# Performance work log

Measured on AMD Instinct MI355X. Metric: run time of the kernel, lower is better.

Reference implementation:

```python
import jax, jax.numpy as jnp
import numpy as np
import math

B, T, C, N = 2, 2048, 1024, 16  # batch, seq, h_dim, n_heads
D = C // N                      # head dim = 64


def setup_inputs() -> dict:
    key = jax.random.key(0)
    ks = jax.random.split(key, 9)
    s = 1.0 / math.sqrt(C)
    x = jax.random.normal(ks[0], (B, T, C), dtype=jnp.float32)
    Wq = jax.random.normal(ks[1], (C, C), dtype=jnp.float32) * s
    Wk = jax.random.normal(ks[2], (C, C), dtype=jnp.float32) * s
    Wv = jax.random.normal(ks[3], (C, C), dtype=jnp.float32) * s
    Wp = jax.random.normal(ks[4], (C, C), dtype=jnp.float32) * s
    bq = jax.random.normal(ks[5], (C,), dtype=jnp.float32) * 0.01
    bk = jax.random.normal(ks[6], (C,), dtype=jnp.float32) * 0.01
    bv = jax.random.normal(ks[7], (C,), dtype=jnp.float32) * 0.01
    bp = jax.random.normal(ks[8], (C,), dtype=jnp.float32) * 0.01
    mask = jnp.tril(jnp.ones((T, T), dtype=jnp.int32))[None, None]  # [1,1,T,T] causal
    return {"x": x, "Wq": Wq, "bq": bq, "Wk": Wk, "bk": bk,
            "Wv": Wv, "bv": bv, "Wp": Wp, "bp": bp, "mask": mask}


def reference(x, Wq, bq, Wk, bk, Wv, bv, Wp, bp, mask):
    b, t, c = x.shape
    n, d = N, c // N
    # projections; rearrange 'b t (n d) -> b n t d'
    q = (x @ Wq + bq).reshape(b, t, n, d).transpose(0, 2, 1, 3)
    k = (x @ Wk + bk).reshape(b, t, n, d).transpose(0, 2, 1, 3)
    v = (x @ Wv + bv).reshape(b, t, n, d).transpose(0, 2, 1, 3)
    # source: (q @ k^T).transpose(2,3) -> weights[b,n,i,j] = q_j . k_i (TRANSPOSED scores)
    weights = jnp.einsum('bntd,bnsd->bnst', q, k) / math.sqrt(d)
    weights = jnp.where(mask == 0, -jnp.inf, weights)
    attn = jax.nn.softmax(weights, axis=-1)          # softmax over query index j
    out = jnp.einsum('bnij,bnjd->bnid', attn, v)     # [b,n,t,d]
    out = out.transpose(0, 2, 1, 3).reshape(b, t, c)
    return out @ Wp + bp
```

## Files before the change

### kernel.cpp

```cpp
#include <hip/hip_runtime.h>
#include <hip/hip_bf16.h>

#define TT 2048

typedef __attribute__((ext_vector_type(8))) short bf16x8;
typedef __attribute__((ext_vector_type(4))) float f32x4;
typedef __attribute__((ext_vector_type(8))) unsigned short us8;
typedef __attribute__((ext_vector_type(4))) unsigned short us4;

typedef __attribute__((address_space(1))) void gvoid;
typedef __attribute__((address_space(3))) void svoid;

__device__ __forceinline__ void gll16(const void* g, void* l) {
    __builtin_amdgcn_global_load_lds((gvoid*)g, (svoid*)l, 16, 0, 0);
}

__device__ __forceinline__ unsigned short f2bf(float f) {
    union { float f; unsigned u; } v; v.f = f;
    unsigned r = v.u + 0x7fffu + ((v.u >> 16) & 1u);
    return (unsigned short)(r >> 16);
}
__device__ __forceinline__ float bf2f(unsigned short u) {
    union { unsigned u; float f; } v; v.u = ((unsigned)u) << 16;
    return v.f;
}

#define MFMA16(a, b, c) __builtin_amdgcn_mfma_f32_16x16x32_bf16((a), (b), (c), 0, 0, 0)

__global__ __launch_bounds__(256) void convert_x(const float* __restrict__ x,
                                                 unsigned short* __restrict__ xh,
                                                 unsigned short* __restrict__ xl) {
    const int i = blockIdx.x * 256 + threadIdx.x;
    const float4 a = ((const float4*)x)[2 * i];
    const float4 b = ((const float4*)x)[2 * i + 1];
    const float v[8] = {a.x, a.y, a.z, a.w, b.x, b.y, b.z, b.w};
    us8 H, L;
    #pragma unroll
    for (int j = 0; j < 8; ++j) {
        const unsigned short h = f2bf(v[j]);
        H[j] = h;
        L[j] = f2bf(v[j] - bf2f(h));
    }
    ((us8*)xh)[i] = H;
    ((us8*)xl)[i] = L;
}

__global__ __launch_bounds__(256) void convert_w(const float* __restrict__ W,
                                                 unsigned short* __restrict__ Wh,
                                                 unsigned short* __restrict__ Wl) {
    __shared__ float tile[32 * 33];
    const int t = threadIdx.x;
    const int k0 = blockIdx.x * 32, n0 = blockIdx.y * 32;

    const int kl_ = t >> 3, nc = (t & 7) * 4;
    const float4 v = *(const float4*)&W[(size_t)(k0 + kl_) * 1024 + n0 + nc];
    tile[(nc + 0) * 33 + kl_] = v.x;
    tile[(nc + 1) * 33 + kl_] = v.y;
    tile[(nc + 2) * 33 + kl_] = v.z;
    tile[(nc + 3) * 33 + kl_] = v.w;
    __syncthreads();
    const int nl = t >> 3, kc = (t & 7) * 4;
    us4 H, L;
    #pragma unroll
    for (int j = 0; j < 4; ++j) {
        const float f = tile[nl * 33 + kc + j];
        const unsigned short h = f2bf(f);
        H[j] = h;
        L[j] = f2bf(f - bf2f(h));
    }
    *(us4*)&Wh[(size_t)(n0 + nl) * 1024 + k0 + kc] = H;
    *(us4*)&Wl[(size_t)(n0 + nl) * 1024 + k0 + kc] = L;
}

template <int BM, int OUTMODE>
__global__ __launch_bounds__(256, 2)
void proj2(const unsigned short* __restrict__ Ah, const unsigned short* __restrict__ Al,
           const unsigned short* __restrict__ Bh, const unsigned short* __restrict__ Bl,
           const float* __restrict__ bias0, const float* __restrict__ bias1,
           unsigned short* __restrict__ Oh, unsigned short* __restrict__ Ol,
           float* __restrict__ Of) {
    constexpr int MT = BM / 32;
    constexpr int RW = BM / 2;
    constexpr int CA = BM / 64;
    __shared__ __align__(16) unsigned short sm[BM * 64 + 8192];
    unsigned short* sAh = sm;
    unsigned short* sAl = sm + BM * 32;
    unsigned short* sBh = sm + BM * 64;
    unsigned short* sBl = sm + BM * 64 + 4096;

    const int t = threadIdx.x;
    const int lane = t & 63, w = t >> 6;
    const int wr = w >> 1, wc = w & 1;
    const int l15 = lane & 15, lq = lane >> 4;

    const int nwg = gridDim.x * gridDim.y;
    const int bid = blockIdx.y * gridDim.x + blockIdx.x;
    const int swz = (bid & 7) * (nwg >> 3) + (bid >> 3);
    const int bx = swz % gridDim.x, by = swz / gridDim.x;
    const int row0 = bx * BM;
    const int col0 = by * 128;

    f32x4 acc[MT][4] = {};

    for (int k0 = 0; k0 < 1024; k0 += 32) {
        __syncthreads();
        #pragma unroll
        for (int cc = 0; cc < CA; ++cc) {
            const int c = w * CA + cc;
            const int r = c * 16 + (lane >> 2);
            const int src = (row0 + r) * 1024 + k0 + 8 * ((lane & 3) ^ ((r >> 1) & 3));
            gll16(&Ah[src], &sAh[c * 512]);
            gll16(&Al[src], &sAl[c * 512]);
        }
        #pragma unroll
        for (int cc = 0; cc < 2; ++cc) {
            const int c = w * 2 + cc;
            const int r = c * 16 + (lane >> 2);
            const int src = (col0 + r) * 1024 + k0 + 8 * ((lane & 3) ^ ((r >> 1) & 3));
            gll16(&Bh[src], &sBh[c * 512]);
            gll16(&Bl[src], &sBl[c * 512]);
        }
        __syncthreads();

        bf16x8 aH[MT], aL[MT], bH[4], bL[4];
        #pragma unroll
        for (int nt = 0; nt < 4; ++nt) {
            const int rn = 64 * wc + 16 * nt + l15;
            const int off = rn * 32 + 8 * (lq ^ ((rn >> 1) & 3));
            bH[nt] = *(const bf16x8*)&sBh[off];
            bL[nt] = *(const bf16x8*)&sBl[off];
        }
        #pragma unroll
        for (int mt = 0; mt < MT; ++mt) {
            const int rm = RW * wr + 16 * mt + l15;
            const int off = rm * 32 + 8 * (lq ^ ((rm >> 1) & 3));
            aH[mt] = *(const bf16x8*)&sAh[off];
            aL[mt] = *(const bf16x8*)&sAl[off];
        }
        #pragma unroll
        for (int mt = 0; mt < MT; ++mt)
            #pragma unroll
            for (int nt = 0; nt < 4; ++nt) {
                acc[mt][nt] = MFMA16(aH[mt], bH[nt], acc[mt][nt]);
                acc[mt][nt] = MFMA16(aH[mt], bL[nt], acc[mt][nt]);
                acc[mt][nt] = MFMA16(aL[mt], bH[nt], acc[mt][nt]);
            }
    }

    if (OUTMODE == 3) {
        __syncthreads();
        unsigned short* sv = sm;
        #pragma unroll
        for (int mt = 0; mt < MT; ++mt)
            #pragma unroll
            for (int nt = 0; nt < 4; ++nt) {
                const int cl = 64 * wc + 16 * nt + l15;
                const float bb = bias0[col0 + cl];
                #pragma unroll
                for (int r = 0; r < 4; ++r) {
                    const int tl = RW * wr + 16 * mt + 4 * lq + r;
                    sv[cl * 72 + tl] = f2bf(acc[mt][nt][r] + bb);
                }
            }
        __syncthreads();
        const int b = row0 >> 11, t0 = row0 & 2047;
        #pragma unroll
        for (int it = 0; it < 4; ++it) {
            const int cl = it * 32 + (t >> 3);
            const int ts = (t & 7) * 8;
            const us8 o8 = *(const us8*)&sv[cl * 72 + ts];
            const int c = col0 + cl;
            *(us8*)&Oh[((size_t)((b * 16 + (c >> 6)) * 64 + (c & 63))) * 2048 + t0 + ts] = o8;
        }
        return;
    }

    __syncthreads();
    float* sc = (float*)sm + w * (RW * 32);
    #pragma unroll
    for (int h = 0; h < 2; ++h) {
        #pragma unroll
        for (int mt = 0; mt < MT; ++mt)
            #pragma unroll
            for (int nt2 = 0; nt2 < 2; ++nt2) {
                const int nt = 2 * h + nt2;
                const int colg = col0 + 64 * wc + 16 * nt + l15;
                float bb;
                if (OUTMODE == 0) bb = (col0 < 1024) ? bias0[colg] : bias1[colg - 1024];
                else bb = bias0[colg];
                const int cl = 16 * nt2 + l15;
                #pragma unroll
                for (int r = 0; r < 4; ++r) {
                    const int row = 16 * mt + 4 * lq + r;
                    sc[row * 32 + 4 * ((cl >> 2) ^ (row & 7)) + (cl & 3)] = acc[mt][nt][r] + bb;
                }
            }
        asm volatile("" ::: "memory");
        #pragma unroll
        for (int it = 0; it < RW / 16; ++it) {
            const int rl = it * 16 + (lane >> 2);
            const int c8 = (lane & 3) * 8;
            const float4 f0 = *(const float4*)&sc[rl * 32 + 4 * ((c8 >> 2) ^ (rl & 7))];
            const float4 f1 = *(const float4*)&sc[rl * 32 + 4 * (((c8 >> 2) + 1) ^ (rl & 7))];
            const int gr = row0 + RW * wr + rl;
            const int gc = col0 + 64 * wc + 32 * h + c8;
            if (OUTMODE == 2) {
                *(float4*)&Of[(size_t)gr * 1024 + gc] = f0;
                *(float4*)&Of[(size_t)gr * 1024 + gc + 4] = f1;
            } else {
                const float v[8] = {f0.x, f0.y, f0.z, f0.w, f1.x, f1.y, f1.z, f1.w};
                us8 H, L;
                #pragma unroll
                for (int j = 0; j < 8; ++j) {
                    const unsigned short hh = f2bf(v[j]);
                    H[j] = hh;
                    L[j] = f2bf(v[j] - bf2f(hh));
                }
                *(us8*)&Oh[(size_t)gr * 2048 + gc] = H;
                *(us8*)&Ol[(size_t)gr * 2048 + gc] = L;
            }
        }
        asm volatile("" ::: "memory");
    }
}

__global__ __launch_bounds__(256, 2)
void attn2(const unsigned short* __restrict__ QKh, const unsigned short* __restrict__ QKl,
           const unsigned short* __restrict__ Vt,
           unsigned short* __restrict__ Oh, unsigned short* __restrict__ Ol) {
    __shared__ __align__(16) unsigned short sm[20480];
    unsigned short* sQh = sm;
    unsigned short* sQl = sm + 4096;
    unsigned short* sKh = sm + 8192;
    unsigned short* sKl = sm + 12288;
    unsigned short* sVt = sm + 16384;
    unsigned short* sP  = sm;

    const int t = threadIdx.x;
    const int lane = t & 63, w = t >> 6;
    const int l15 = lane & 15, lq = lane >> 4;
    const int bn = blockIdx.x;
    const int b = bn >> 4, n = bn & 15;
    const int qt = (gridDim.y - 1) - blockIdx.y;
    const int rowQ0 = b * TT + qt * 64;
    const int colQ = 1024 + n * 64;
    const int colK = n * 64;

    #pragma unroll
    for (int cc = 0; cc < 2; ++cc) {
        const int c = w * 2 + cc;
        const int r = 8 * c + (lane >> 3);
        const int src = (rowQ0 + r) * 2048 + colQ + 8 * ((lane & 7) ^ (r & 7));
        gll16(&QKh[src], &sQh[c * 512]);
        gll16(&QKl[src], &sQl[c * 512]);
    }
    __syncthreads();
    bf16x8 qH[2], qL[2];
    #pragma unroll
    for (int kh = 0; kh < 2; ++kh) {
        const int rq = 16 * w + l15;
        const int off = rq * 64 + 8 * ((lq + 4 * kh) ^ (rq & 7));
        qH[kh] = *(const bf16x8*)&sQh[off];
        qL[kh] = *(const bf16x8*)&sQl[off];
    }

    float m_[4], l_[4];
    f32x4 o[4] = {};
    #pragma unroll
    for (int r = 0; r < 4; ++r) { m_[r] = -1e30f; l_[r] = 0.f; }

    for (int kt = 0; kt <= qt; ++kt) {
        const int rowK0 = b * TT + kt * 64;
        __syncthreads();
        #pragma unroll
        for (int cc = 0; cc < 2; ++cc) {
            const int c = w * 2 + cc;
            const int r = 8 * c + (lane >> 3);
            const int src = (rowK0 + r) * 2048 + colK + 8 * ((lane & 7) ^ (r & 7));
            gll16(&QKh[src], &sKh[c * 512]);
            gll16(&QKl[src], &sKl[c * 512]);
        }
        #pragma unroll
        for (int cc = 0; cc < 2; ++cc) {
            const int c = w * 2 + cc;
            const int r = 8 * c + (lane >> 3);
            const int src = (bn * 64 + r) * 2048 + kt * 64 + 8 * ((lane & 7) ^ (r & 7));
            gll16(&Vt[src], &sVt[c * 512]);
        }
        __syncthreads();

        f32x4 s[4] = {};
        const int njt = (kt == qt) ? (w + 1) : 4;
        __builtin_amdgcn_s_setprio(1);
        #pragma unroll
        for (int kh = 0; kh < 2; ++kh) {
            #pragma unroll
            for (int jt = 0; jt < 4; ++jt) {
                if (jt >= njt) continue;
                const int rk = 16 * jt + l15;
                const int offk = rk * 64 + 8 * ((lq + 4 * kh) ^ (rk & 7));
                const bf16x8 kH = *(const bf16x8*)&sKh[offk];
                const bf16x8 kL = *(const bf16x8*)&sKl[offk];
                s[jt] = MFMA16(qH[kh], kH, s[jt]);
                s[jt] = MFMA16(qH[kh], kL, s[jt]);
                s[jt] = MFMA16(qL[kh], kH, s[jt]);
            }
        }
        __builtin_amdgcn_s_setprio(0);
        if (kt == qt) {
            #pragma unroll
            for (int jt = 0; jt < 4; ++jt)
                #pragma unroll
                for (int r = 0; r < 4; ++r)
                    if (16 * jt + l15 > 16 * w + 4 * lq + r) s[jt][r] = -1e30f;
        }

        float mx[4];
        int need = 0;
        #pragma unroll
        for (int r = 0; r < 4; ++r) {
            float m0 = fmaxf(fmaxf(s[0][r], s[1][r]), fmaxf(s[2][r], s[3][r]));
            #pragma unroll
            for (int off = 8; off; off >>= 1) m0 = fmaxf(m0, __shfl_xor(m0, off, 16));
            mx[r] = m0;
            need |= (m0 > m_[r] + 16.f) ? 1 : 0;
        }
        float po[4][4];
        if (__any(need)) {
            #pragma unroll
            for (int r = 0; r < 4; ++r) {
                const float mnew = fmaxf(m_[r], mx[r]);
                const float alpha = __expf((m_[r] - mnew) * 0.125f);
                m_[r] = mnew;
                float ps = 0.f;
                #pragma unroll
                for (int jt = 0; jt < 4; ++jt) {
                    const float p = __expf((s[jt][r] - mnew) * 0.125f);
                    po[r][jt] = p;
                    ps += p;
                }
                #pragma unroll
                for (int off = 8; off; off >>= 1) ps += __shfl_xor(ps, off, 16);
                l_[r] = l_[r] * alpha + ps;
                #pragma unroll
                for (int dt = 0; dt < 4; ++dt) o[dt][r] *= alpha;
            }
        } else {
            #pragma unroll
            for (int r = 0; r < 4; ++r) {
                float ps = 0.f;
                #pragma unroll
                for (int jt = 0; jt < 4; ++jt) {
                    const float p = __expf((s[jt][r] - m_[r]) * 0.125f);
                    po[r][jt] = p;
                    ps += p;
                }
                #pragma unroll
                for (int off = 8; off; off >>= 1) ps += __shfl_xor(ps, off, 16);
                l_[r] += ps;
            }
        }
        unsigned short* Pw = sP + w * 1024;
        #pragma unroll
        for (int r = 0; r < 4; ++r) {
            const int rl = 4 * lq + r;
            #pragma unroll
            for (int jt = 0; jt < 4; ++jt) {
                const int c = 16 * jt + l15;
                Pw[rl * 64 + 8 * ((c >> 3) ^ (rl & 7)) + (c & 7)] = f2bf(po[r][jt]);
            }
        }
        __syncthreads();

        __builtin_amdgcn_s_setprio(1);
        #pragma unroll
        for (int kh = 0; kh < 2; ++kh) {
            const int offp = l15 * 64 + 8 * ((lq + 4 * kh) ^ (l15 & 7));
            const bf16x8 pa = *(const bf16x8*)&Pw[offp];
            #pragma unroll
            for (int dt = 0; dt < 4; ++dt) {
                const int rd = 16 * dt + l15;
                const int offv = rd * 64 + 8 * ((lq + 4 * kh) ^ (rd & 7));
                const bf16x8 vb = *(const bf16x8*)&sVt[offv];
                o[dt] = MFMA16(pa, vb, o[dt]);
            }
        }
        __builtin_amdgcn_s_setprio(0);
    }

    __syncthreads();
    float inv[4];
    #pragma unroll
    for (int r = 0; r < 4; ++r) inv[r] = 1.0f / l_[r];
    float* sc = (float*)sm + w * (16 * 68);
    #pragma unroll
    for (int dt = 0; dt < 4; ++dt)
        #pragma unroll
        for (int r = 0; r < 4; ++r)
            sc[(4 * lq + r) * 68 + 16 * dt + l15] = o[dt][r] * inv[r];
    asm volatile("" ::: "memory");
    #pragma unroll
    for (int it = 0; it < 2; ++it) {
        const int rl = 8 * it + (lane >> 3);
        const int c8 = (lane & 7) * 8;
        const float4 f0 = *(const float4*)&sc[rl * 68 + c8];
        const float4 f1 = *(const float4*)&sc[rl * 68 + c8 + 4];
        const float v[8] = {f0.x, f0.y, f0.z, f0.w, f1.x, f1.y, f1.z, f1.w};
        us8 H, L;
        #pragma unroll
        for (int j = 0; j < 8; ++j) {
            const unsigned short h = f2bf(v[j]);
            H[j] = h;
            L[j] = f2bf(v[j] - bf2f(h));
        }
        const int gt = rowQ0 + 16 * w + rl;
        *(us8*)&Oh[(size_t)gt * 1024 + (n * 64) + c8] = H;
        *(us8*)&Ol[(size_t)gt * 1024 + (n * 64) + c8] = L;
    }
}

extern "C" void kernel_launch(void* const* d_in, const int* in_sizes, int n_in,
                              void* d_out, int out_size, void* d_ws, size_t ws_size,
                              hipStream_t stream) {
    const float* x  = (const float*)d_in[0];
    const float* Wq = (const float*)d_in[1];
    const float* bq = (const float*)d_in[2];
    const float* Wk = (const float*)d_in[3];
    const float* bk = (const float*)d_in[4];
    const float* Wv = (const float*)d_in[5];
    const float* bv = (const float*)d_in[6];
    const float* Wp = (const float*)d_in[7];
    const float* bp = (const float*)d_in[8];
    float* out = (float*)d_out;

    char* p = (char*)d_ws;
    const size_t MB = 1024 * 1024;
    unsigned short* xh  = (unsigned short*)(p);
    unsigned short* xl  = (unsigned short*)(p +  8 * MB);
    unsigned short* qkh = (unsigned short*)(p + 16 * MB);
    unsigned short* qkl = (unsigned short*)(p + 32 * MB);
    unsigned short* vh  = (unsigned short*)(p + 48 * MB);
    unsigned short* wbh = (unsigned short*)(p + 56 * MB);
    unsigned short* wbl = (unsigned short*)(p + 60 * MB);
    unsigned short* wsh = (unsigned short*)(p + 56 * MB);
    unsigned short* wsl = (unsigned short*)(p + 58 * MB);
    unsigned short* oh = xh;
    unsigned short* ol = xl;

    const dim3 blk(256);
    const dim3 gw(32, 32);

    convert_x<<<2048, blk, 0, stream>>>(x, xh, xl);

    convert_w<<<gw, blk, 0, stream>>>(Wq, wbh, wbl);
    convert_w<<<gw, blk, 0, stream>>>(Wk, wbh + 1024 * 1024, wbl + 1024 * 1024);
    proj2<128, 0><<<dim3(32, 16), blk, 0, stream>>>(xh, xl, wbh, wbl, bq, bk,
                                                    qkh, qkl, nullptr);
    convert_w<<<gw, blk, 0, stream>>>(Wv, wsh, wsl);
    proj2<64, 3><<<dim3(64, 8), blk, 0, stream>>>(xh, xl, wsh, wsl, bv, nullptr,
                                                  vh, nullptr, nullptr);

    attn2<<<dim3(32, 32), blk, 0, stream>>>(qkh, qkl, vh, oh, ol);

    convert_w<<<gw, blk, 0, stream>>>(Wp, wsh, wsl);
    proj2<64, 2><<<dim3(64, 8), blk, 0, stream>>>(oh, ol, wsh, wsl, bp, nullptr,
                                                  nullptr, nullptr, out);
}
```

Before: 316.6 us.

## Double-buffer LDS staging in projection GEMM and attention K/V loop

Both the projection GEMM and the attention kernel now use two LDS buffers. The next K-slice or K/V tile is issued with global_load_lds while the current one is consumed by MFMAs, and only one barrier per iteration remains instead of two. The attention kernel also drops the barrier before the P·V step, since each wave reads back only its own P region, and the GEMM raises wave priority around its MFMA block. This is meant to hide global-memory latency behind compute, at the cost of doubling LDS use, which could limit occupancy.

Measured after the change: 312.3 us. No clear change (-1.4%).

```diff
diff --git a/kernel.cpp b/kernel.cpp
--- a/kernel.cpp
+++ b/kernel.cpp
@@ -82,11 +82,8 @@
     constexpr int MT = BM / 32;
     constexpr int RW = BM / 2;
     constexpr int CA = BM / 64;
-    __shared__ __align__(16) unsigned short sm[BM * 64 + 8192];
-    unsigned short* sAh = sm;
-    unsigned short* sAl = sm + BM * 32;
-    unsigned short* sBh = sm + BM * 64;
-    unsigned short* sBl = sm + BM * 64 + 4096;
+    constexpr int BUFU = BM * 64 + 8192;
+    __shared__ __align__(16) unsigned short sm[2 * BUFU];
 
     const int t = threadIdx.x;
     const int lane = t & 63, w = t >> 6;
@@ -100,43 +97,51 @@
     const int row0 = bx * BM;
     const int col0 = by * 128;
 
-    f32x4 acc[MT][4] = {};
-
-    for (int k0 = 0; k0 < 1024; k0 += 32) {
-        __syncthreads();
+    auto stage = [&](int k0, unsigned short* base) {
         #pragma unroll
         for (int cc = 0; cc < CA; ++cc) {
             const int c = w * CA + cc;
             const int r = c * 16 + (lane >> 2);
             const int src = (row0 + r) * 1024 + k0 + 8 * ((lane & 3) ^ ((r >> 1) & 3));
-            gll16(&Ah[src], &sAh[c * 512]);
-            gll16(&Al[src], &sAl[c * 512]);
+            gll16(&Ah[src], &base[c * 512]);
+            gll16(&Al[src], &base[BM * 32 + c * 512]);
         }
         #pragma unroll
         for (int cc = 0; cc < 2; ++cc) {
             const int c = w * 2 + cc;
             const int r = c * 16 + (lane >> 2);
             const int src = (col0 + r) * 1024 + k0 + 8 * ((lane & 3) ^ ((r >> 1) & 3));
-            gll16(&Bh[src], &sBh[c * 512]);
-            gll16(&Bl[src], &sBl[c * 512]);
-        }
-        __syncthreads();
+            gll16(&Bh[src], &base[BM * 64 + c * 512]);
+            gll16(&Bl[src], &base[BM * 64 + 4096 + c * 512]);
+        }
+    };
+
+    f32x4 acc[MT][4] = {};
+
+    stage(0, sm);
+    __syncthreads();
+    int cur = 0;
+
+    for (int k0 = 0; k0 < 1024; k0 += 32) {
+        unsigned short* base = sm + cur * BUFU;
+        if (k0 + 32 < 1024) stage(k0 + 32, sm + (cur ^ 1) * BUFU);
 
         bf16x8 aH[MT], aL[MT], bH[4], bL[4];
         #pragma unroll
         for (int nt = 0; nt < 4; ++nt) {
             const int rn = 64 * wc + 16 * nt + l15;
             const int off = rn * 32 + 8 * (lq ^ ((rn >> 1) & 3));
-            bH[nt] = *(const bf16x8*)&sBh[off];
-            bL[nt] = *(const bf16x8*)&sBl[off];
+            bH[nt] = *(const bf16x8*)&base[BM * 64 + off];
+            bL[nt] = *(const bf16x8*)&base[BM * 64 + 4096 + off];
         }
         #pragma unroll
         for (int mt = 0; mt < MT; ++mt) {
             const int rm = RW * wr + 16 * mt + l15;
             const int off = rm * 32 + 8 * (lq ^ ((rm >> 1) & 3));
-            aH[mt] = *(const bf16x8*)&sAh[off];
-            aL[mt] = *(const bf16x8*)&sAl[off];
-        }
+            aH[mt] = *(const bf16x8*)&base[off];
+            aL[mt] = *(const bf16x8*)&base[BM * 32 + off];
+        }
+        __builtin_amdgcn_s_setprio(1);
         #pragma unroll
         for (int mt = 0; mt < MT; ++mt)
             #pragma unroll
@@ -145,10 +150,12 @@
                 acc[mt][nt] = MFMA16(aH[mt], bL[nt], acc[mt][nt]);
                 acc[mt][nt] = MFMA16(aL[mt], bH[nt], acc[mt][nt]);
             }
+        __builtin_amdgcn_s_setprio(0);
+        __syncthreads();
+        cur ^= 1;
     }
 
     if (OUTMODE == 3) {
-        __syncthreads();
         unsigned short* sv = sm;
         #pragma unroll
         for (int mt = 0; mt < MT; ++mt)
@@ -175,7 +182,6 @@
         return;
     }
 
-    __syncthreads();
     float* sc = (float*)sm + w * (RW * 32);
     #pragma unroll
     for (int h = 0; h < 2; ++h) {
@@ -228,12 +234,10 @@
 void attn2(const unsigned short* __restrict__ QKh, const unsigned short* __restrict__ QKl,
            const unsigned short* __restrict__ Vt,
            unsigned short* __restrict__ Oh, unsigned short* __restrict__ Ol) {
-    __shared__ __align__(16) unsigned short sm[20480];
+    constexpr int BUFU = 12288;
+    __shared__ __align__(16) unsigned short sm[8192 + 2 * BUFU];
     unsigned short* sQh = sm;
     unsigned short* sQl = sm + 4096;
-    unsigned short* sKh = sm + 8192;
-    unsigned short* sKl = sm + 12288;
-    unsigned short* sVt = sm + 16384;
     unsigned short* sP  = sm;
 
     const int t = threadIdx.x;
@@ -246,6 +250,25 @@
     const int colQ = 1024 + n * 64;
     const int colK = n * 64;
 
+    auto stageKV = [&](int kt, unsigned short* base) {
+        const int rowK0 = b * TT + kt * 64;
+        #pragma unroll
+        for (int cc = 0; cc < 2; ++cc) {
+            const int c = w * 2 + cc;
+            const int r = 8 * c + (lane >> 3);
+            const int src = (rowK0 + r) * 2048 + colK + 8 * ((lane & 7) ^ (r & 7));
+            gll16(&QKh[src], &base[c * 512]);
+            gll16(&QKl[src], &base[4096 + c * 512]);
+        }
+        #pragma unroll
+        for (int cc = 0; cc < 2; ++cc) {
+            const int c = w * 2 + cc;
+            const int r = 8 * c + (lane >> 3);
+            const int src = (bn * 64 + r) * 2048 + kt * 64 + 8 * ((lane & 7) ^ (r & 7));
+            gll16(&Vt[src], &base[8192 + c * 512]);
+        }
+    };
+
     #pragma unroll
     for (int cc = 0; cc < 2; ++cc) {
         const int c = w * 2 + cc;
@@ -254,7 +277,9 @@
         gll16(&QKh[src], &sQh[c * 512]);
         gll16(&QKl[src], &sQl[c * 512]);
     }
+    stageKV(0, sm + 8192);
     __syncthreads();
+
     bf16x8 qH[2], qL[2];
     #pragma unroll
     for (int kh = 0; kh < 2; ++kh) {
@@ -269,25 +294,10 @@
     #pragma unroll
     for (int r = 0; r < 4; ++r) { m_[r] = -1e30f; l_[r] = 0.f; }
 
+    int cur = 0;
     for (int kt = 0; kt <= qt; ++kt) {
-        const int rowK0 = b * TT + kt * 64;
-        __syncthreads();
-        #pragma unroll
-        for (int cc = 0; cc < 2; ++cc) {
-            const int c = w * 2 + cc;
-            const int r = 8 * c + (lane >> 3);
-            const int src = (rowK0 + r) * 2048 + colK + 8 * ((lane & 7) ^ (r & 7));
-            gll16(&QKh[src], &sKh[c * 512]);
-            gll16(&QKl[src], &sKl[c * 512]);
-        }
-        #pragma unroll
-        for (int cc = 0; cc < 2; ++cc) {
-            const int c = w * 2 + cc;
-            const int r = 8 * c + (lane >> 3);
-            const int src = (bn * 64 + r) * 2048 + kt * 64 + 8 * ((lane & 7) ^ (r & 7));
-            gll16(&Vt[src], &sVt[c * 512]);
-        }
-        __syncthreads();
+        unsigned short* base = sm + 8192 + cur * BUFU;
+        if (kt < qt) stageKV(kt + 1, sm + 8192 + (cur ^ 1) * BUFU);
 
         f32x4 s[4] = {};
         const int njt = (kt == qt) ? (w + 1) : 4;
@@ -299,8 +309,8 @@
                 if (jt >= njt) continue;
                 const int rk = 16 * jt + l15;
                 const int offk = rk * 64 + 8 * ((lq + 4 * kh) ^ (rk & 7));
-                const bf16x8 kH = *(const bf16x8*)&sKh[offk];
-                const bf16x8 kL = *(const bf16x8*)&sKl[offk];
+                const bf16x8 kH = *(const bf16x8*)&base[offk];
+                const bf16x8 kL = *(const bf16x8*)&base[4096 + offk];
                 s[jt] = MFMA16(qH[kh], kH, s[jt]);
                 s[jt] = MFMA16(qH[kh], kL, s[jt]);
                 s[jt] = MFMA16(qL[kh], kH, s[jt]);
@@ -370,7 +380,6 @@
                 Pw[rl * 64 + 8 * ((c >> 3) ^ (rl & 7)) + (c & 7)] = f2bf(po[r][jt]);
             }
         }
-        __syncthreads();
 
         __builtin_amdgcn_s_setprio(1);
         #pragma unroll
@@ -381,14 +390,16 @@
             for (int dt = 0; dt < 4; ++dt) {
                 const int rd = 16 * dt + l15;
                 const int offv = rd * 64 + 8 * ((lq + 4 * kh) ^ (rd & 7));
-                const bf16x8 vb = *(const bf16x8*)&sVt[offv];
+                const bf16x8 vb = *(const bf16x8*)&base[8192 + offv];
                 o[dt] = MFMA16(pa, vb, o[dt]);
             }
         }
         __builtin_amdgcn_s_setprio(0);
-    }
-
-    __syncthreads();
+
+        __syncthreads();
+        cur ^= 1;
+    }
+
     float inv[4];
     #pragma unroll
     for (int r = 0; r < 4; ++r) inv[r] = 1.0f / l_[r];
```
